# Optimization experiments

Measured on AMD Instinct MI355X. Metric: run time of the kernel, lower is better.

The kernel has to match this reference:

```python
import jax, jax.numpy as jnp
import numpy as np

NUM_INPUTS = 376
NUM_ACTIONS = 17
L1, L2 = 256, 128
BHID = 128
NE = 2
B = 65536


def setup_inputs() -> dict:
    key = jax.random.key(0)
    ks = jax.random.split(key, 16)
    s = lambda k, shape: jax.random.normal(k, shape, dtype=jnp.float32) * 0.05
    return {
        "states": jax.random.normal(ks[0], (B, NUM_INPUTS), dtype=jnp.float32),
        # blending module params
        "bw1": s(ks[1], (BHID, NUM_INPUTS)), "bb1": s(ks[2], (BHID,)),
        "bw2": s(ks[3], (BHID, BHID)),       "bb2": s(ks[4], (BHID,)),
        "bwo": s(ks[5], (NE, BHID)),         "bbo": s(ks[6], (NE,)),
        # stacked expert (p1, p2) policy params, leading axis = expert
        "ew1": s(ks[7], (NE, L1, NUM_INPUTS)), "eb1": s(ks[8], (NE, L1)),
        "ew2": s(ks[9], (NE, L2, L1)),         "eb2": s(ks[10], (NE, L2)),
        "ewm": s(ks[11], (NE, NUM_ACTIONS, L2)), "ebm": s(ks[12], (NE, NUM_ACTIONS)),
    }


def _blended_linear(h, coeffs, W, b):
    # Linear with per-sample blended weights: (sum_e c_e W_e) h + sum_e c_e b_e
    # == sum_e c_e (W_e h + b_e), so compute both expert outputs and blend.
    y = jnp.einsum('bi,eoi->beo', h, W) + b[None]  # [B, E, O]
    return jnp.einsum('be,beo->bo', coeffs, y)


def reference(states, bw1, bb1, bw2, bb2, bwo, bbo, ew1, eb1, ew2, eb2, ewm, ebm):
    # BlendingModule: 2-layer relu MLP -> softmax over experts
    g = jax.nn.relu(states @ bw1.T + bb1)
    g = jax.nn.relu(g @ bw2.T + bb2)
    coeffs = jax.nn.softmax(g @ bwo.T + bbo, axis=-1)  # [B, 2]
    # Per-sample blended PolicyModule (256 -> 128 -> actions, tanh head)
    h = jax.nn.relu(_blended_linear(states, coeffs, ew1, eb1))
    h = jax.nn.relu(_blended_linear(h, coeffs, ew2, eb2))
    mu = jnp.tanh(_blended_linear(h, coeffs, ewm, ebm))
    return mu
```

## Files before the change

kernel.cpp:

```cpp
#include <hip/hip_runtime.h>
#include <math.h>


typedef __attribute__((ext_vector_type(8))) _Float16 half8;
typedef __attribute__((ext_vector_type(4))) _Float16 half4;
typedef __attribute__((ext_vector_type(4))) float    f32x4;

#define MFMA16(a, b, c) __builtin_amdgcn_mfma_f32_16x16x32_f16((a), (b), (c), 0, 0, 0)
#define SWZ(row) (((row) & 7) << 4)

#define MT 64
#define T  512

#define S_B   0
#define G_B   49152
#define H1_B  49152
#define H2_B  49152
#define LDS_BYTES 81920

#define WS_W1 0
#define WS_W2 49152
#define WS_E1 65536
#define WS_E2 262144
#define WS_EM 327680
#define WS_HALFS 335872
#define WS_BYTES 671744

__device__ __forceinline__ half8 cvt8(const float* __restrict__ p) {
    const float4 a = *reinterpret_cast<const float4*>(p);
    const float4 b = *reinterpret_cast<const float4*>(p + 4);
    half8 r;
    r[0] = (_Float16)a.x; r[1] = (_Float16)a.y; r[2] = (_Float16)a.z; r[3] = (_Float16)a.w;
    r[4] = (_Float16)b.x; r[5] = (_Float16)b.y; r[6] = (_Float16)b.z; r[7] = (_Float16)b.w;
    return r;
}

__global__ __launch_bounds__(256)
void prep_weights(const float* __restrict__ bw1, const float* __restrict__ bb1,
                  const float* __restrict__ bw2,
                  const float* __restrict__ ew1, const float* __restrict__ eb1,
                  const float* __restrict__ ew2,
                  const float* __restrict__ ewm, _Float16* __restrict__ wsw)
{
    const int i = blockIdx.x * 256 + threadIdx.x;
    if (i >= WS_HALFS) return;
    int sec; const float* W; const float* Bv; int N, K, KC, j0;
    if      (i < 49152)  { sec = 0; W = bw1; Bv = bb1;     N = 128; K = 376; KC = 12; j0 = i - WS_W1; }
    else if (i < 65536)  { sec = 1; W = bw2; Bv = nullptr; N = 128; K = 128; KC = 4;  j0 = i - WS_W2; }
    else if (i < 262144) { sec = 2; W = ew1; Bv = eb1;     N = 512; K = 376; KC = 12; j0 = i - WS_E1; }
    else if (i < 327680) { sec = 3; W = ew2; Bv = nullptr; N = 256; K = 256; KC = 8;  j0 = i - WS_E2; }
    else                 { sec = 4; W = ewm; Bv = nullptr; N = 34;  K = 128; KC = 4;  j0 = i - WS_EM; }
    const int tile = j0 >> 9;
    const int rem  = j0 & 511;
    const int l    = rem >> 3;
    const int jj   = rem & 7;
    const int n0   = tile / KC, kc = tile - n0 * KC;
    const int n = n0 * 16 + (l & 15);
    const int k = kc * 32 + (l >> 4) * 8 + jj;
    float v = 0.f;
    if (sec == 4) {
        const int e = n >> 5, a = n & 31;
        if (a < 17 && k < K) v = ewm[(e * 17 + a) * K + k];
    } else if (n < N) {
        if (k < K)             v = W[n * K + k];
        else if (k == K && Bv) v = Bv[n];
    }
    wsw[i] = (_Float16)v;
}

template <bool USE_WS>
__global__ __launch_bounds__(512)
__attribute__((amdgpu_waves_per_eu(2)))
void actor_kernel(const float* __restrict__ states,
                  const float* __restrict__ bw1, const float* __restrict__ bb1,
                  const float* __restrict__ bw2, const float* __restrict__ bb2,
                  const float* __restrict__ bwo, const float* __restrict__ bbo,
                  const float* __restrict__ ew1, const float* __restrict__ eb1,
                  const float* __restrict__ ew2, const float* __restrict__ eb2,
                  const float* __restrict__ ewm, const float* __restrict__ ebm,
                  const _Float16* __restrict__ wsw,
                  float* __restrict__ out)
{
    extern __shared__ char smc[];
    const int t    = threadIdx.x;
    const int l    = t & 63;
    const int l15  = l & 15;
    const int kgrp = l >> 4;
    const int kg16 = kgrp * 16;
    const int wv   = __builtin_amdgcn_readfirstlane(t >> 6);
    const int base = blockIdx.x * MT;
    const int lB   = l * 8;

    const half8 zf = {0,0,0,0,0,0,0,0};

    {
        const float4* src = reinterpret_cast<const float4*>(states + (long)base * 376);
        for (int q = t; q < MT * 94; q += T) {
            const int r  = q / 94;
            const int c4 = q - r * 94;
            const float4 v = src[q];
            half4 h;
            h[0] = (_Float16)v.x; h[1] = (_Float16)v.y;
            h[2] = (_Float16)v.z; h[3] = (_Float16)v.w;
            *(half4*)(smc + S_B + ((r * 768 + c4 * 8) ^ SWZ(r))) = h;
        }
        if (t < MT) {
            const int off = (t * 768 + 752) ^ SWZ(t);
            *(ushort4*)(smc + S_B + off)     = make_ushort4(0x3C00u, 0, 0, 0);
            *(ushort4*)(smc + S_B + off + 8) = make_ushort4(0, 0, 0, 0);
        }
    }
    __syncthreads();

    {
        f32x4 acc[4] = {{0,0,0,0},{0,0,0,0},{0,0,0,0},{0,0,0,0}};
        const int col = wv * 16 + l15;
        auto ldW = [&](int kc) -> half8 {
            if constexpr (USE_WS) return *(const half8*)(wsw + WS_W1 + (wv * 12 + kc) * 512 + lB);
            else {
                const int g = kc * 4 + kgrp;
                if (g < 47) return cvt8(bw1 + col * 376 + g * 8);
                half8 rr = zf; rr[0] = (_Float16)bb1[col]; return rr;
            }
        };
        half8 bf = ldW(0);
        #pragma unroll
        for (int kc = 0; kc < 12; ++kc) {
            const half8 cur = bf;
            if (kc < 11) bf = ldW(kc + 1);
            const int koff = kc * 64 + kg16;
            #pragma unroll
            for (int mt = 0; mt < 4; ++mt) {
                const int row = mt * 16 + l15;
                const half8 af = *(const half8*)(smc + S_B + ((row * 768 + koff) ^ SWZ(row)));
                acc[mt] = MFMA16(af, cur, acc[mt]);
            }
        }
        #pragma unroll
        for (int mt = 0; mt < 4; ++mt) {
            #pragma unroll
            for (int j = 0; j < 4; ++j) {
                const int row = mt * 16 + kgrp * 4 + j;
                const float v = fmaxf(acc[mt][j], 0.f);
                *(_Float16*)(smc + G_B + ((row * 256 + col * 2) ^ SWZ(row))) = (_Float16)v;
            }
        }
    }
    __syncthreads();

    {
        f32x4 acc[4] = {{0,0,0,0},{0,0,0,0},{0,0,0,0},{0,0,0,0}};
        const int col = wv * 16 + l15;
        auto ldW = [&](int kc) -> half8 {
            if constexpr (USE_WS) return *(const half8*)(wsw + WS_W2 + (wv * 4 + kc) * 512 + lB);
            else                  return cvt8(bw2 + col * 128 + (kc * 4 + kgrp) * 8);
        };
        half8 bf = ldW(0);
        #pragma unroll
        for (int kc = 0; kc < 4; ++kc) {
            const half8 cur = bf;
            if (kc < 3) bf = ldW(kc + 1);
            const int koff = kc * 64 + kg16;
            #pragma unroll
            for (int mt = 0; mt < 4; ++mt) {
                const int row = mt * 16 + l15;
                const half8 af = *(const half8*)(smc + G_B + ((row * 256 + koff) ^ SWZ(row)));
                acc[mt] = MFMA16(af, cur, acc[mt]);
            }
        }
        __syncthreads();
        const float bias = bb2[col];
        #pragma unroll
        for (int mt = 0; mt < 4; ++mt) {
            #pragma unroll
            for (int j = 0; j < 4; ++j) {
                const int row = mt * 16 + kgrp * 4 + j;
                const float v = fmaxf(acc[mt][j] + bias, 0.f);
                *(_Float16*)(smc + G_B + ((row * 256 + col * 2) ^ SWZ(row))) = (_Float16)v;
            }
        }
    }
    __syncthreads();

    {
        const int s     = t >> 3;
        const int r     = t & 7;
        const int e     = r & 1;
        const int chunk = r >> 1;
        float z = 0.f;
        const float* wo = bwo + e * 128 + chunk * 32;
        #pragma unroll
        for (int q = 0; q < 4; ++q) {
            const half8 hv = *(const half8*)(smc + G_B + ((s * 256 + chunk * 64 + q * 16) ^ SWZ(s)));
            const float4 w0 = *(const float4*)(wo + q * 8);
            const float4 w1 = *(const float4*)(wo + q * 8 + 4);
            z = fmaf((float)hv[0], w0.x, z); z = fmaf((float)hv[1], w0.y, z);
            z = fmaf((float)hv[2], w0.z, z); z = fmaf((float)hv[3], w0.w, z);
            z = fmaf((float)hv[4], w1.x, z); z = fmaf((float)hv[5], w1.y, z);
            z = fmaf((float)hv[6], w1.z, z); z = fmaf((float)hv[7], w1.w, z);
        }
        z += __shfl_xor(z, 2, 64);
        z += __shfl_xor(z, 4, 64);
        z += bbo[e];
        const float zo = __shfl_xor(z, 1, 64);
        if (r < 2) {
            const float m = fmaxf(z, zo);
            const float ea = __expf(z - m), eb = __expf(zo - m);
            const float c_self = ea / (ea + eb);
            const _Float16 ch = (_Float16)c_self;
            const _Float16 cl = (_Float16)(c_self - (float)ch);
            union { _Float16 h[2]; unsigned u; } pk;
            pk.h[0] = ch; pk.h[1] = cl;
            *(unsigned*)(smc + S_B + (((s * 768 + 752) ^ SWZ(s)) + 8 + e * 4)) = pk.u;
        }
    }
    __syncthreads();

    #pragma unroll
    for (int p = 0; p < 2; ++p) {
        f32x4 aA[4], aB[4];
        #pragma unroll
        for (int mt = 0; mt < 4; ++mt) { aA[mt] = {0,0,0,0}; aB[mt] = {0,0,0,0}; }
        auto ldE1 = [&](int kc, int ex) -> half8 {
            if constexpr (USE_WS) {
                const int n0 = wv * 2 + p + ex * 16;
                return *(const half8*)(wsw + WS_E1 + (n0 * 12 + kc) * 512 + lB);
            } else {
                const int g = kc * 4 + kgrp;
                const int wr = wv * 32 + p * 16 + l15 + ex * 256;
                if (g < 47) return cvt8(ew1 + wr * 376 + g * 8);
                half8 rr = zf; rr[0] = (_Float16)eb1[wr]; return rr;
            }
        };
        half8 b0 = ldE1(0, 0), b1 = ldE1(0, 1);
        #pragma unroll
        for (int kc = 0; kc < 12; ++kc) {
            const half8 c0f = b0, c1f = b1;
            if (kc < 11) { b0 = ldE1(kc + 1, 0); b1 = ldE1(kc + 1, 1); }
            const int koff = kc * 64 + kg16;
            #pragma unroll
            for (int mt = 0; mt < 4; ++mt) {
                const int row = mt * 16 + l15;
                const half8 af = *(const half8*)(smc + S_B + ((row * 768 + koff) ^ SWZ(row)));
                aA[mt] = MFMA16(af, c0f, aA[mt]);
                aB[mt] = MFMA16(af, c1f, aB[mt]);
            }
        }
        const int col = wv * 32 + p * 16 + l15;
        #pragma unroll
        for (int mt = 0; mt < 4; ++mt) {
            #pragma unroll
            for (int j = 0; j < 4; ++j) {
                const int row = mt * 16 + kgrp * 4 + j;
                const half4 cc = *(const half4*)(smc + S_B + (((row * 768 + 752) ^ SWZ(row)) + 8));
                const float c0 = (float)cc[0] + (float)cc[1];
                const float c1 = (float)cc[2] + (float)cc[3];
                const float v = fmaxf(c0 * aA[mt][j] + c1 * aB[mt][j], 0.f);
                *(_Float16*)(smc + H1_B + ((row * 512 + col * 2) ^ SWZ(row))) = (_Float16)v;
            }
        }
    }
    __syncthreads();

    {
        f32x4 cA[4], cB[4];
        #pragma unroll
        for (int mt = 0; mt < 4; ++mt) { cA[mt] = {0,0,0,0}; cB[mt] = {0,0,0,0}; }
        const int col = wv * 16 + l15;
        auto ldE2 = [&](int kc, int ex) -> half8 {
            if constexpr (USE_WS) {
                return *(const half8*)(wsw + WS_E2 + ((wv + ex * 8) * 8 + kc) * 512 + lB);
            } else {
                const int g = kc * 4 + kgrp;
                return cvt8(ew2 + (col + ex * 128) * 256 + g * 8);
            }
        };
        half8 b0 = ldE2(0, 0), b1 = ldE2(0, 1);
        #pragma unroll
        for (int kc = 0; kc < 8; ++kc) {
            const half8 c0f = b0, c1f = b1;
            if (kc < 7) { b0 = ldE2(kc + 1, 0); b1 = ldE2(kc + 1, 1); }
            const int koff = kc * 64 + kg16;
            #pragma unroll
            for (int mt = 0; mt < 4; ++mt) {
                const int row = mt * 16 + l15;
                const half8 af = *(const half8*)(smc + H1_B + ((row * 512 + koff) ^ SWZ(row)));
                cA[mt] = MFMA16(af, c0f, cA[mt]);
                cB[mt] = MFMA16(af, c1f, cB[mt]);
            }
        }
        __syncthreads();
        const float b0s = eb2[col], b1s = eb2[128 + col];
        #pragma unroll
        for (int mt = 0; mt < 4; ++mt) {
            #pragma unroll
            for (int j = 0; j < 4; ++j) {
                const int row = mt * 16 + kgrp * 4 + j;
                const half4 cc = *(const half4*)(smc + S_B + (((row * 768 + 752) ^ SWZ(row)) + 8));
                const float c0 = (float)cc[0] + (float)cc[1];
                const float c1 = (float)cc[2] + (float)cc[3];
                const float v = fmaxf(c0 * (cA[mt][j] + b0s) + c1 * (cB[mt][j] + b1s), 0.f);
                *(_Float16*)(smc + H2_B + ((row * 256 + col * 2) ^ SWZ(row))) = (_Float16)v;
            }
        }
    }
    __syncthreads();

    {
        const int colt = wv & 1;
        const int mtq  = wv >> 1;
        f32x4 c0a = {0,0,0,0}, c1a = {0,0,0,0};
        const int col  = colt * 16 + l15;
        const bool vcol = (col < 17);
        const int arow = mtq * 16 + l15;
        for (int kc = 0; kc < 4; ++kc) {
            const int koff = kc * 64 + kg16;
            const half8 af = *(const half8*)(smc + H2_B + ((arow * 256 + koff) ^ SWZ(arow)));
            half8 b0, b1;
            if constexpr (USE_WS) {
                b0 = *(const half8*)(wsw + WS_EM + (colt * 4 + kc) * 512 + lB);
                b1 = *(const half8*)(wsw + WS_EM + ((2 + colt) * 4 + kc) * 512 + lB);
            } else {
                const int g = kc * 4 + kgrp;
                b0 = vcol ? cvt8(ewm + col * 128 + g * 8)        : zf;
                b1 = vcol ? cvt8(ewm + (17 + col) * 128 + g * 8) : zf;
            }
            c0a = MFMA16(af, b0, c0a);
            c1a = MFMA16(af, b1, c1a);
        }
        if (vcol) {
            const float b0 = ebm[col], b1 = ebm[17 + col];
            #pragma unroll
            for (int j = 0; j < 4; ++j) {
                const int row = mtq * 16 + kgrp * 4 + j;
                const half4 cc = *(const half4*)(smc + S_B + (((row * 768 + 752) ^ SWZ(row)) + 8));
                const float c0 = (float)cc[0] + (float)cc[1];
                const float c1 = (float)cc[2] + (float)cc[3];
                const float z = c0 * (c0a[j] + b0) + c1 * (c1a[j] + b1);
                const float e2x = __expf(2.f * z);
                out[(long)(base + row) * 17 + col] = 1.f - 2.f / (e2x + 1.f);
            }
        }
    }
}

extern "C" void kernel_launch(void* const* d_in, const int* in_sizes, int n_in,
                              void* d_out, int out_size, void* d_ws, size_t ws_size,
                              hipStream_t stream) {
    (void)in_sizes; (void)n_in; (void)out_size;
    const float* states = (const float*)d_in[0];
    const float* bw1 = (const float*)d_in[1];
    const float* bb1 = (const float*)d_in[2];
    const float* bw2 = (const float*)d_in[3];
    const float* bb2 = (const float*)d_in[4];
    const float* bwo = (const float*)d_in[5];
    const float* bbo = (const float*)d_in[6];
    const float* ew1 = (const float*)d_in[7];
    const float* eb1 = (const float*)d_in[8];
    const float* ew2 = (const float*)d_in[9];
    const float* eb2 = (const float*)d_in[10];
    const float* ewm = (const float*)d_in[11];
    const float* ebm = (const float*)d_in[12];
    float* out = (float*)d_out;

    const int nblk = 65536 / MT;

    if (d_ws != nullptr && ws_size >= (size_t)WS_BYTES) {
        _Float16* wsw = (_Float16*)d_ws;
        prep_weights<<<dim3((WS_HALFS + 255) / 256), dim3(256), 0, stream>>>(
            bw1, bb1, bw2, ew1, eb1, ew2, ewm, wsw);
        actor_kernel<true><<<dim3(nblk), dim3(T), LDS_BYTES, stream>>>(
            states, bw1, bb1, bw2, bb2, bwo, bbo,
            ew1, eb1, ew2, eb2, ewm, ebm, wsw, out);
    } else {
        actor_kernel<false><<<dim3(nblk), dim3(T), LDS_BYTES, stream>>>(
            states, bw1, bb1, bw2, bb2, bwo, bbo,
            ew1, eb1, ew2, eb2, ewm, ebm, nullptr, out);
    }
}
```

Baseline: 98.12 us.

## Double block size to 1024 threads and split MFMA tiles across more waves

Measured after the change: 87.95 us. 1.12x faster.

```diff
diff --git a/kernel.cpp b/kernel.cpp
--- a/kernel.cpp
+++ b/kernel.cpp
@@ -10,7 +10,7 @@
 #define SWZ(row) (((row) & 7) << 4)
 
 #define MT 64
-#define T  512
+#define T  1024
 
 #define S_B   0
 #define G_B   49152
@@ -69,8 +69,8 @@
 }
 
 template <bool USE_WS>
-__global__ __launch_bounds__(512)
-__attribute__((amdgpu_waves_per_eu(2)))
+__global__ __launch_bounds__(1024)
+__attribute__((amdgpu_waves_per_eu(4, 4)))
 void actor_kernel(const float* __restrict__ states,
                   const float* __restrict__ bw1, const float* __restrict__ bb1,
                   const float* __restrict__ bw2, const float* __restrict__ bb2,
@@ -113,10 +113,11 @@
     __syncthreads();
 
     {
-        f32x4 acc[4] = {{0,0,0,0},{0,0,0,0},{0,0,0,0},{0,0,0,0}};
-        const int col = wv * 16 + l15;
+        const int ng = wv >> 1, mh = wv & 1;
+        f32x4 acc[2] = {{0,0,0,0},{0,0,0,0}};
+        const int col = ng * 16 + l15;
         auto ldW = [&](int kc) -> half8 {
-            if constexpr (USE_WS) return *(const half8*)(wsw + WS_W1 + (wv * 12 + kc) * 512 + lB);
+            if constexpr (USE_WS) return *(const half8*)(wsw + WS_W1 + (ng * 12 + kc) * 512 + lB);
             else {
                 const int g = kc * 4 + kgrp;
                 if (g < 47) return cvt8(bw1 + col * 376 + g * 8);
@@ -130,17 +131,17 @@
             if (kc < 11) bf = ldW(kc + 1);
             const int koff = kc * 64 + kg16;
             #pragma unroll
-            for (int mt = 0; mt < 4; ++mt) {
-                const int row = mt * 16 + l15;
+            for (int mt = 0; mt < 2; ++mt) {
+                const int row = mh * 32 + mt * 16 + l15;
                 const half8 af = *(const half8*)(smc + S_B + ((row * 768 + koff) ^ SWZ(row)));
                 acc[mt] = MFMA16(af, cur, acc[mt]);
             }
         }
         #pragma unroll
-        for (int mt = 0; mt < 4; ++mt) {
-            #pragma unroll
-            for (int j = 0; j < 4; ++j) {
-                const int row = mt * 16 + kgrp * 4 + j;
+        for (int mt = 0; mt < 2; ++mt) {
+            #pragma unroll
+            for (int j = 0; j < 4; ++j) {
+                const int row = mh * 32 + mt * 16 + kgrp * 4 + j;
                 const float v = fmaxf(acc[mt][j], 0.f);
                 *(_Float16*)(smc + G_B + ((row * 256 + col * 2) ^ SWZ(row))) = (_Float16)v;
             }
@@ -149,10 +150,11 @@
     __syncthreads();
 
     {
-        f32x4 acc[4] = {{0,0,0,0},{0,0,0,0},{0,0,0,0},{0,0,0,0}};
-        const int col = wv * 16 + l15;
+        const int ng = wv >> 1, mh = wv & 1;
+        f32x4 acc[2] = {{0,0,0,0},{0,0,0,0}};
+        const int col = ng * 16 + l15;
         auto ldW = [&](int kc) -> half8 {
-            if constexpr (USE_WS) return *(const half8*)(wsw + WS_W2 + (wv * 4 + kc) * 512 + lB);
+            if constexpr (USE_WS) return *(const half8*)(wsw + WS_W2 + (ng * 4 + kc) * 512 + lB);
             else                  return cvt8(bw2 + col * 128 + (kc * 4 + kgrp) * 8);
         };
         half8 bf = ldW(0);
@@ -162,8 +164,8 @@
             if (kc < 3) bf = ldW(kc + 1);
             const int koff = kc * 64 + kg16;
             #pragma unroll
-            for (int mt = 0; mt < 4; ++mt) {
-                const int row = mt * 16 + l15;
+            for (int mt = 0; mt < 2; ++mt) {
+                const int row = mh * 32 + mt * 16 + l15;
                 const half8 af = *(const half8*)(smc + G_B + ((row * 256 + koff) ^ SWZ(row)));
                 acc[mt] = MFMA16(af, cur, acc[mt]);
             }
@@ -171,10 +173,10 @@
         __syncthreads();
         const float bias = bb2[col];
         #pragma unroll
-        for (int mt = 0; mt < 4; ++mt) {
-            #pragma unroll
-            for (int j = 0; j < 4; ++j) {
-                const int row = mt * 16 + kgrp * 4 + j;
+        for (int mt = 0; mt < 2; ++mt) {
+            #pragma unroll
+            for (int j = 0; j < 4; ++j) {
+                const int row = mh * 32 + mt * 16 + kgrp * 4 + j;
                 const float v = fmaxf(acc[mt][j] + bias, 0.f);
                 *(_Float16*)(smc + G_B + ((row * 256 + col * 2) ^ SWZ(row))) = (_Float16)v;
             }
@@ -183,15 +185,15 @@
     __syncthreads();
 
     {
-        const int s     = t >> 3;
-        const int r     = t & 7;
+        const int s     = t >> 4;
+        const int r     = t & 15;
         const int e     = r & 1;
         const int chunk = r >> 1;
         float z = 0.f;
-        const float* wo = bwo + e * 128 + chunk * 32;
-        #pragma unroll
-        for (int q = 0; q < 4; ++q) {
-            const half8 hv = *(const half8*)(smc + G_B + ((s * 256 + chunk * 64 + q * 16) ^ SWZ(s)));
+        const float* wo = bwo + e * 128 + chunk * 16;
+        #pragma unroll
+        for (int q = 0; q < 2; ++q) {
+            const half8 hv = *(const half8*)(smc + G_B + ((s * 256 + chunk * 32 + q * 16) ^ SWZ(s)));
             const float4 w0 = *(const float4*)(wo + q * 8);
             const float4 w1 = *(const float4*)(wo + q * 8 + 4);
             z = fmaf((float)hv[0], w0.x, z); z = fmaf((float)hv[1], w0.y, z);
@@ -201,6 +203,7 @@
         }
         z += __shfl_xor(z, 2, 64);
         z += __shfl_xor(z, 4, 64);
+        z += __shfl_xor(z, 8, 64);
         z += bbo[e];
         const float zo = __shfl_xor(z, 1, 64);
         if (r < 2) {
@@ -216,18 +219,18 @@
     }
     __syncthreads();
 
-    #pragma unroll
-    for (int p = 0; p < 2; ++p) {
+    {
         f32x4 aA[4], aB[4];
         #pragma unroll
         for (int mt = 0; mt < 4; ++mt) { aA[mt] = {0,0,0,0}; aB[mt] = {0,0,0,0}; }
+        const int col = wv * 16 + l15;
         auto ldE1 = [&](int kc, int ex) -> half8 {
             if constexpr (USE_WS) {
-                const int n0 = wv * 2 + p + ex * 16;
+                const int n0 = wv + ex * 16;
                 return *(const half8*)(wsw + WS_E1 + (n0 * 12 + kc) * 512 + lB);
             } else {
                 const int g = kc * 4 + kgrp;
-                const int wr = wv * 32 + p * 16 + l15 + ex * 256;
+                const int wr = col + ex * 256;
                 if (g < 47) return cvt8(ew1 + wr * 376 + g * 8);
                 half8 rr = zf; rr[0] = (_Float16)eb1[wr]; return rr;
             }
@@ -246,7 +249,6 @@
                 aB[mt] = MFMA16(af, c1f, aB[mt]);
             }
         }
-        const int col = wv * 32 + p * 16 + l15;
         #pragma unroll
         for (int mt = 0; mt < 4; ++mt) {
             #pragma unroll
@@ -263,13 +265,14 @@
     __syncthreads();
 
     {
-        f32x4 cA[4], cB[4];
-        #pragma unroll
-        for (int mt = 0; mt < 4; ++mt) { cA[mt] = {0,0,0,0}; cB[mt] = {0,0,0,0}; }
-        const int col = wv * 16 + l15;
+        const int nt2 = wv & 7, mh = wv >> 3;
+        f32x4 cA[2], cB[2];
+        #pragma unroll
+        for (int mt = 0; mt < 2; ++mt) { cA[mt] = {0,0,0,0}; cB[mt] = {0,0,0,0}; }
+        const int col = nt2 * 16 + l15;
         auto ldE2 = [&](int kc, int ex) -> half8 {
             if constexpr (USE_WS) {
-                return *(const half8*)(wsw + WS_E2 + ((wv + ex * 8) * 8 + kc) * 512 + lB);
+                return *(const half8*)(wsw + WS_E2 + ((nt2 + ex * 8) * 8 + kc) * 512 + lB);
             } else {
                 const int g = kc * 4 + kgrp;
                 return cvt8(ew2 + (col + ex * 128) * 256 + g * 8);
@@ -282,8 +285,8 @@
             if (kc < 7) { b0 = ldE2(kc + 1, 0); b1 = ldE2(kc + 1, 1); }
             const int koff = kc * 64 + kg16;
             #pragma unroll
-            for (int mt = 0; mt < 4; ++mt) {
-                const int row = mt * 16 + l15;
+            for (int mt = 0; mt < 2; ++mt) {
+                const int row = mh * 32 + mt * 16 + l15;
                 const half8 af = *(const half8*)(smc + H1_B + ((row * 512 + koff) ^ SWZ(row)));
                 cA[mt] = MFMA16(af, c0f, cA[mt]);
                 cB[mt] = MFMA16(af, c1f, cB[mt]);
@@ -292,10 +295,10 @@
         __syncthreads();
         const float b0s = eb2[col], b1s = eb2[128 + col];
         #pragma unroll
-        for (int mt = 0; mt < 4; ++mt) {
-            #pragma unroll
-            for (int j = 0; j < 4; ++j) {
-                const int row = mt * 16 + kgrp * 4 + j;
+        for (int mt = 0; mt < 2; ++mt) {
+            #pragma unroll
+            for (int j = 0; j < 4; ++j) {
+                const int row = mh * 32 + mt * 16 + kgrp * 4 + j;
                 const half4 cc = *(const half4*)(smc + S_B + (((row * 768 + 752) ^ SWZ(row)) + 8));
                 const float c0 = (float)cc[0] + (float)cc[1];
                 const float c1 = (float)cc[2] + (float)cc[3];
@@ -306,7 +309,7 @@
     }
     __syncthreads();
 
-    {
+    if (wv < 8) {
         const int colt = wv & 1;
         const int mtq  = wv >> 1;
         f32x4 c0a = {0,0,0,0}, c1a = {0,0,0,0};
```
